# Performance work log

Measured on AMD Instinct MI355X. Metric: run time of the kernel, lower is better.

Reference implementation:

```python
import jax, jax.numpy as jnp
import numpy as np

N, E, IN, HID, OUT = 50000, 800000, 128, 96, 2


def setup_inputs() -> dict:
    key = jax.random.key(0)
    ks = jax.random.split(key, 10)
    x = jax.random.normal(ks[0], (N, IN), jnp.float32)
    edge_index = jax.random.randint(ks[1], (2, E), 0, N, dtype=jnp.int64)
    # PQVA mask: per-node, first output channel is a "known" quantity (masked out),
    # second is the prediction target -> ~mask selects exactly N elements.
    m = np.zeros((N, OUT), dtype=bool)
    m[:, 0] = True
    PQVA_mask = jnp.asarray(m)
    scaler_mean = 0.1 * jax.random.normal(ks[2], (IN,), jnp.float32)
    scaler_std = 0.5 + jax.random.uniform(ks[3], (IN,), jnp.float32)  # in [0.5, 1.5)
    W1 = jax.random.normal(ks[4], (IN, HID), jnp.float32) / np.sqrt(IN)
    W2 = jax.random.normal(ks[5], (HID, HID), jnp.float32) / np.sqrt(HID)
    W3 = jax.random.normal(ks[6], (HID, HID), jnp.float32) / np.sqrt(HID)
    Wout = jax.random.normal(ks[7], (HID, OUT), jnp.float32) / np.sqrt(HID)
    b1 = jnp.zeros((HID,), jnp.float32)
    b2 = jnp.zeros((HID,), jnp.float32)
    b3 = jnp.zeros((HID,), jnp.float32)
    bout = jnp.zeros((OUT,), jnp.float32)
    return {"x": x, "edge_index": edge_index, "PQVA_mask": PQVA_mask,
            "scaler_mean": scaler_mean, "scaler_std": scaler_std,
            "W1": W1, "b1": b1, "W2": W2, "b2": b2, "W3": W3, "b3": b3,
            "Wout": Wout, "bout": bout}


def reference(x, edge_index, PQVA_mask, scaler_mean, scaler_std,
              W1, b1, W2, b2, W3, b3, Wout, bout):
    n = x.shape[0]
    loop = jnp.arange(n, dtype=edge_index.dtype)
    src = jnp.concatenate([edge_index[0], loop])  # add self-loops (GCNConv default)
    dst = jnp.concatenate([edge_index[1], loop])
    deg = jax.ops.segment_sum(jnp.ones_like(dst, x.dtype), dst, num_segments=n)
    dinv = jax.lax.rsqrt(deg)  # deg >= 1 thanks to self-loops
    norm = (dinv[src] * dinv[dst])[:, None]  # [E+N, 1]

    def prop(h):  # D^-1/2 (A+I) D^-1/2 @ h  via gather-scale-scatter
        return jax.ops.segment_sum(h[src] * norm, dst, num_segments=n)

    h = (x - scaler_mean) / scaler_std          # standard scaler
    h = jax.nn.relu(prop(h @ W1) + b1)          # GCNConv 1 + ReLU
    h = jax.nn.relu(prop(h @ W2) + b2)          # GCNConv 2 + ReLU
    h = prop(h @ W3) + b3                       # GCNConv 3 (last, no act)
    out = h @ Wout + bout                       # final Linear -> [N, OUT]
    # masked reshape: ~mask has exactly one True per node -> [N]
    return out.reshape(-1)[~PQVA_mask.reshape(-1)]
```

## Files before the change

### kernel.cpp

```cpp
#include <hip/hip_runtime.h>
#include <hip/hip_fp16.h>

#define IN_F 128
#define HID_F 96
#define PB 512
#define MAXB 8192

typedef _Float16 f16x8 __attribute__((ext_vector_type(8)));
typedef float f32x4 __attribute__((ext_vector_type(4)));


__device__ __forceinline__ void swizzle_one(const float* W, __half* Wsw, int idx) {
    int j  = idx & 7;
    int ln = (idx >> 3) & 63;
    int ct = idx >> 9;
    int t = ct % 6, c = ct / 6;
    int k   = c * 32 + (ln >> 4) * 8 + j;
    int col = t * 16 + (ln & 15);
    Wsw[idx] = (__half)W[k * 96 + col];
}

__global__ __launch_bounds__(256) void prep_kernel(
        const float* __restrict__ stdv, float* __restrict__ rstd,
        const float* __restrict__ W3, const float* __restrict__ Wout,
        const float* __restrict__ b3, const float* __restrict__ bout,
        float* __restrict__ wv, float* __restrict__ cconst,
        int* __restrict__ bhist,
        const float* __restrict__ W1, __half* __restrict__ Wsw1, int SW1,
        const float* __restrict__ W2, __half* __restrict__ Wsw2, int SW2) {
    int b = blockIdx.x, t = threadIdx.x;
    if (b == 0) {
        bhist[t] = 0;
        if (t < IN_F) rstd[t] = 1.0f / stdv[t];
        if (t < HID_F) {
            float s = 0.f;
            for (int j = 0; j < HID_F; ++j) s += W3[t * HID_F + j] * Wout[j * 2 + 1];
            wv[t] = s;
        }
        if (t == 0) {
            float s = 0.f;
            for (int j = 0; j < HID_F; ++j) s += b3[j] * Wout[j * 2 + 1];
            cconst[0] = s + bout[1];
        }
    } else if (b <= 48) {
        int idx = (b - 1) * 256 + t;
        if (idx < SW1) swizzle_one(W1, Wsw1, idx);
    } else {
        int idx = (b - 49) * 256 + t;
        if (idx < SW2) swizzle_one(W2, Wsw2, idx);
    }
}


__global__ __launch_bounds__(256) void hist_kernel(const int* __restrict__ dstv,
                                                   int* __restrict__ bhist, int E) {
    __shared__ int h[256];
    int t = threadIdx.x;
    h[t] = 0;
    __syncthreads();
    int i = blockIdx.x * 256 + t;
    int stride = gridDim.x * 256;
    for (int e = i; e < E; e += stride) atomicAdd(&h[dstv[e] >> 8], 1);
    __syncthreads();
    int v = h[t];
    if (v) atomicAdd(&bhist[t], v);
}

__global__ __launch_bounds__(256) void bucket_scan_kernel(const int* __restrict__ bhist,
                                                          int* __restrict__ base,
                                                          int* __restrict__ bcur) {
    __shared__ int tmp[256];
    int t = threadIdx.x;
    int v = bhist[t];
    tmp[t] = v;
    __syncthreads();
#pragma unroll
    for (int off = 1; off < 256; off <<= 1) {
        int u = (t >= off) ? tmp[t - off] : 0;
        __syncthreads();
        tmp[t] += u;
        __syncthreads();
    }
    int ex = tmp[t] - v;
    base[t] = ex;
    bcur[t] = ex;
}

__global__ __launch_bounds__(256) void partition_kernel(
        const int* __restrict__ srcv, const int* __restrict__ dstv,
        int* __restrict__ bcur, int* __restrict__ ebuf, int E) {
    __shared__ int h[256];
    __shared__ int cur[256];
    int t = threadIdx.x;
    int chunk = (E + PB - 1) / PB;
    int s = blockIdx.x * chunk;
    int eend = min(s + chunk, E);
    h[t] = 0;
    __syncthreads();
    for (int e = s + t; e < eend; e += 256) atomicAdd(&h[dstv[e] >> 8], 1);
    __syncthreads();
    if (h[t]) cur[t] = atomicAdd(&bcur[t], h[t]);
    __syncthreads();
    for (int e = s + t; e < eend; e += 256) {
        int sv = srcv[e], d = dstv[e];
        int p = atomicAdd(&cur[d >> 8], 1);
        ebuf[p] = (sv << 8) | (d & 255);
    }
}

__global__ __launch_bounds__(256) void buildcsr_kernel(
        const int* __restrict__ ebuf, const int* __restrict__ base,
        const int* __restrict__ bhist, int* __restrict__ rowoff,
        float* __restrict__ dinv, int* __restrict__ cols, int n, int E) {
    __shared__ int dg[256];
    __shared__ int tmp[256];
    __shared__ int cur[256];
    __shared__ int colst[MAXB];
    int t = threadIdx.x;
    int k = blockIdx.x;
    int seg = base[k], cnt = bhist[k];
    dg[t] = 0;
    __syncthreads();
    for (int i = t; i < cnt; i += 256) atomicAdd(&dg[ebuf[seg + i] & 255], 1);
    __syncthreads();
    int v = dg[t];
    tmp[t] = v;
    __syncthreads();
#pragma unroll
    for (int off = 1; off < 256; off <<= 1) {
        int u = (t >= off) ? tmp[t - off] : 0;
        __syncthreads();
        tmp[t] += u;
        __syncthreads();
    }
    int excl = tmp[t] - v;
    int node = (k << 8) + t;
    if (node < n) {
        rowoff[node] = seg + excl;
        dinv[node] = rsqrtf((float)v + 1.0f);
    }
    if (k == 0 && t == 0) rowoff[n] = E;
    cur[t] = excl;
    __syncthreads();
    if (cnt <= MAXB) {
        for (int i = t; i < cnt; i += 256) {
            int p = ebuf[seg + i];
            int lp = atomicAdd(&cur[p & 255], 1);
            colst[lp] = ((unsigned)p) >> 8;
        }
        __syncthreads();
        for (int i = t; i < cnt; i += 256) cols[seg + i] = colst[i];
    } else {
        for (int i = t; i < cnt; i += 256) {
            int p = ebuf[seg + i];
            int lp = atomicAdd(&cur[p & 255], 1);
            cols[seg + lp] = ((unsigned)p) >> 8;
        }
    }
}


template<int MODE, int K>
__global__ __launch_bounds__(256) void gemm_mfma_kernel(
        const void* __restrict__ Ain, const __half* __restrict__ Wsw,
        const float* __restrict__ mean, const float* __restrict__ rstd,
        const float* __restrict__ dinv, __half* __restrict__ C, int n) {
    constexpr int NCH = K / 32;
    int lane = threadIdx.x & 63;
    int wv_  = threadIdx.x >> 6;
    int m = lane & 15, q = lane >> 4;
    int node0 = blockIdx.x * 64 + wv_ * 16;
    int g = node0 + m;
    int gc = g < n ? g : n - 1;

    f32x4 acc[6];
#pragma unroll
    for (int t = 0; t < 6; ++t) acc[t] = (f32x4){0.f, 0.f, 0.f, 0.f};

#pragma unroll
    for (int c = 0; c < NCH; ++c) {
        f16x8 a;
        if (MODE == 0) {
            const float* ap = (const float*)Ain + (long)gc * K + c * 32 + q * 8;
            float4 v0 = *(const float4*)ap;
            float4 v1 = *(const float4*)(ap + 4);
            float4 m0 = *(const float4*)(mean + c * 32 + q * 8);
            float4 m1 = *(const float4*)(mean + c * 32 + q * 8 + 4);
            float4 r0 = *(const float4*)(rstd + c * 32 + q * 8);
            float4 r1 = *(const float4*)(rstd + c * 32 + q * 8 + 4);
            a[0] = (_Float16)((v0.x - m0.x) * r0.x);
            a[1] = (_Float16)((v0.y - m0.y) * r0.y);
            a[2] = (_Float16)((v0.z - m0.z) * r0.z);
            a[3] = (_Float16)((v0.w - m0.w) * r0.w);
            a[4] = (_Float16)((v1.x - m1.x) * r1.x);
            a[5] = (_Float16)((v1.y - m1.y) * r1.y);
            a[6] = (_Float16)((v1.z - m1.z) * r1.z);
            a[7] = (_Float16)((v1.w - m1.w) * r1.w);
        } else {
            a = *(const f16x8*)((const __half*)Ain + (long)gc * K + c * 32 + q * 8);
        }
#pragma unroll
        for (int t = 0; t < 6; ++t) {
            f16x8 b = *(const f16x8*)(Wsw + (size_t)(((c * 6) + t) * 64 + lane) * 8);
            acc[t] = __builtin_amdgcn_mfma_f32_16x16x32_f16(a, b, acc[t], 0, 0, 0);
        }
    }
    float dv[4];
#pragma unroll
    for (int r = 0; r < 4; ++r) {
        int gr = node0 + q * 4 + r;
        dv[r] = (gr < n) ? dinv[gr] : 0.f;
    }
#pragma unroll
    for (int t = 0; t < 6; ++t)
#pragma unroll
        for (int r = 0; r < 4; ++r) {
            int gr = node0 + q * 4 + r;
            if (gr < n) C[(long)gr * 96 + t * 16 + m] = (__half)(acc[t][r] * dv[r]);
        }
}


template<int DOT>
__global__ __launch_bounds__(256) void prop16_kernel(
        const __half* __restrict__ hin, const int* __restrict__ rowoff,
        const int* __restrict__ cols,
        const float* __restrict__ dinv, const float* __restrict__ bias,
        const float* __restrict__ wvv, __half* __restrict__ hout,
        float* __restrict__ zs, int n) {
    int wid = (blockIdx.x * blockDim.x + threadIdx.x) >> 6;
    int lane = threadIdx.x & 63;
    if (wid >= n) return;
    int e0 = rowoff[wid], e1 = rowoff[wid + 1];
    bool active = lane < 48;
    int g = lane / 12, l = lane - g * 12;
    int gg = active ? g : 0;
    const f16x8* hp = (const f16x8*)hin;

    float acc[8];
#pragma unroll
    for (int j = 0; j < 8; ++j) acc[j] = 0.f;

    int e = e0;
    for (; e + 16 <= e1; e += 16) {
        int c0 = cols[e + gg];
        int c1 = cols[e + 4 + gg];
        int c2 = cols[e + 8 + gg];
        int c3 = cols[e + 12 + gg];
        f16x8 v0 = hp[(long)c0 * 12 + l];
        f16x8 v1 = hp[(long)c1 * 12 + l];
        f16x8 v2 = hp[(long)c2 * 12 + l];
        f16x8 v3 = hp[(long)c3 * 12 + l];
#pragma unroll
        for (int j = 0; j < 8; ++j)
            acc[j] += (float)v0[j] + (float)v1[j] + (float)v2[j] + (float)v3[j];
    }
    for (; e <= e1; e += 4) {
        int idx = e + gg;
        bool isedge = idx < e1;
        int c = wid;
        if (isedge) c = cols[idx];
        f16x8 v = hp[(long)c * 12 + l];
        float fm = (active && idx <= e1) ? 1.f : 0.f;
#pragma unroll
        for (int j = 0; j < 8; ++j) acc[j] += fm * (float)v[j];
    }
#pragma unroll
    for (int j = 0; j < 8; ++j) {
        acc[j] += __shfl_down(acc[j], 24, 64);
        acc[j] += __shfl_down(acc[j], 12, 64);
    }
    float di = dinv[wid];
    if (DOT == 0) {
        if (lane < 12) {
            float4 b0 = *(const float4*)(bias + lane * 8);
            float4 b1 = *(const float4*)(bias + lane * 8 + 4);
            f16x8 o;
            o[0] = (_Float16)fmaxf(di * acc[0] + b0.x, 0.f);
            o[1] = (_Float16)fmaxf(di * acc[1] + b0.y, 0.f);
            o[2] = (_Float16)fmaxf(di * acc[2] + b0.z, 0.f);
            o[3] = (_Float16)fmaxf(di * acc[3] + b0.w, 0.f);
            o[4] = (_Float16)fmaxf(di * acc[4] + b1.x, 0.f);
            o[5] = (_Float16)fmaxf(di * acc[5] + b1.y, 0.f);
            o[6] = (_Float16)fmaxf(di * acc[6] + b1.z, 0.f);
            o[7] = (_Float16)fmaxf(di * acc[7] + b1.w, 0.f);
            *(f16x8*)(hout + (long)wid * 96 + lane * 8) = o;
        }
    } else {
        float v = 0.f;
        if (lane < 12) {
            float4 b0 = *(const float4*)(bias + lane * 8);
            float4 b1 = *(const float4*)(bias + lane * 8 + 4);
            float4 w0 = *(const float4*)(wvv + lane * 8);
            float4 w1 = *(const float4*)(wvv + lane * 8 + 4);
            v  = fmaxf(di * acc[0] + b0.x, 0.f) * w0.x;
            v += fmaxf(di * acc[1] + b0.y, 0.f) * w0.y;
            v += fmaxf(di * acc[2] + b0.z, 0.f) * w0.z;
            v += fmaxf(di * acc[3] + b0.w, 0.f) * w0.w;
            v += fmaxf(di * acc[4] + b1.x, 0.f) * w1.x;
            v += fmaxf(di * acc[5] + b1.y, 0.f) * w1.y;
            v += fmaxf(di * acc[6] + b1.z, 0.f) * w1.z;
            v += fmaxf(di * acc[7] + b1.w, 0.f) * w1.w;
        }
#pragma unroll
        for (int off = 32; off; off >>= 1) v += __shfl_xor(v, off, 64);
        if (lane == 0) zs[wid] = di * v;
    }
}


__global__ __launch_bounds__(256) void prop_scalar_kernel(
        const float* __restrict__ zs, const int* __restrict__ rowoff,
        const int* __restrict__ cols,
        const float* __restrict__ dinv, const float* __restrict__ cconst,
        float* __restrict__ out, int n) {
    int i = blockIdx.x * blockDim.x + threadIdx.x;
    if (i >= n) return;
    int e0 = rowoff[i], e1 = rowoff[i + 1];
    float s = 0.f;
    int e = e0;
    for (; e + 4 <= e1; e += 4) {
        int c0 = cols[e + 0], c1 = cols[e + 1], c2 = cols[e + 2], c3 = cols[e + 3];
        s += zs[c0]; s += zs[c1]; s += zs[c2]; s += zs[c3];
    }
    for (; e < e1; ++e) s += zs[cols[e]];
    out[i] = dinv[i] * (s + zs[i]) + cconst[0];
}


extern "C" void kernel_launch(void* const* d_in, const int* in_sizes, int n_in,
                              void* d_out, int out_size, void* d_ws, size_t ws_size,
                              hipStream_t stream) {
    const float* x    = (const float*)d_in[0];
    const int*   eidx = (const int*)d_in[1];
    const float* mean = (const float*)d_in[3];
    const float* stdv = (const float*)d_in[4];
    const float* W1   = (const float*)d_in[5];
    const float* b1   = (const float*)d_in[6];
    const float* W2   = (const float*)d_in[7];
    const float* b2   = (const float*)d_in[8];
    const float* W3   = (const float*)d_in[9];
    const float* b3   = (const float*)d_in[10];
    const float* Wout = (const float*)d_in[11];
    const float* bout = (const float*)d_in[12];
    float* out = (float*)d_out;

    const int n = in_sizes[0] / IN_F;
    const int E = in_sizes[1] / 2;
    const int* srcv = eidx;
    const int* dstv = eidx + E;
    const int NB = (n + 255) >> 8;

    char* ws = (char*)d_ws;
    size_t off = 0;
    auto alloc = [&](size_t bytes) -> void* {
        void* p = ws + off;
        off = (off + bytes + 255) & ~(size_t)255;
        return p;
    };
    const int SW1 = 4 * 6 * 64 * 8;
    const int SW2 = 3 * 6 * 64 * 8;
    int*    rowoff = (int*)alloc(((size_t)n + 1) * 4);
    float*  dinv   = (float*)alloc((size_t)n * 4);
    int*    cols   = (int*)alloc((size_t)E * 4);
    int*    ebuf   = (int*)alloc((size_t)E * 4);
    int*    bhist  = (int*)alloc(256 * 4);
    int*    base   = (int*)alloc(256 * 4);
    int*    bcur   = (int*)alloc(256 * 4);
    float*  rstd   = (float*)alloc(IN_F * 4);
    float*  wv     = (float*)alloc(HID_F * 4);
    float*  cconst = (float*)alloc(4);
    float*  zbuf   = (float*)alloc((size_t)n * 4);
    __half* Wsw1   = (__half*)alloc((size_t)SW1 * 2);
    __half* Wsw2   = (__half*)alloc((size_t)SW2 * 2);
    __half* bufA   = (__half*)alloc((size_t)n * HID_F * 2);
    __half* bufB   = (__half*)alloc((size_t)n * HID_F * 2);

    prep_kernel<<<85, 256, 0, stream>>>(stdv, rstd, W3, Wout, b3, bout, wv, cconst,
                                        bhist, W1, Wsw1, SW1, W2, Wsw2, SW2);

    hist_kernel<<<256, 256, 0, stream>>>(dstv, bhist, E);
    bucket_scan_kernel<<<1, 256, 0, stream>>>(bhist, base, bcur);
    partition_kernel<<<PB, 256, 0, stream>>>(srcv, dstv, bcur, ebuf, E);
    buildcsr_kernel<<<NB, 256, 0, stream>>>(ebuf, base, bhist, rowoff, dinv, cols, n, E);

    int gemm_grid = (n + 63) / 64;
    int prop_grid = (int)(((long)n * 64 + 255) / 256);

    gemm_mfma_kernel<0, IN_F><<<gemm_grid, 256, 0, stream>>>(x, Wsw1, mean, rstd, dinv,
                                                             bufA, n);
    prop16_kernel<0><<<prop_grid, 256, 0, stream>>>(bufA, rowoff, cols, dinv, b1,
                                                    nullptr, bufB, nullptr, n);
    gemm_mfma_kernel<1, HID_F><<<gemm_grid, 256, 0, stream>>>(bufB, Wsw2, nullptr, nullptr,
                                                              dinv, bufA, n);
    prop16_kernel<1><<<prop_grid, 256, 0, stream>>>(bufA, rowoff, cols, dinv, b2,
                                                    wv, nullptr, zbuf, n);
    prop_scalar_kernel<<<(n + 255) / 256, 256, 0, stream>>>(zbuf, rowoff, cols, dinv,
                                                            cconst, out, n);
}
```

Before: 227.1 us.

## Use fixed-stride bucket slots to drop histogram and scan passes in CSR build

Replaces the histogram, bucket-scan and partition kernels with one partition kernel that writes each destination bucket into a fixed 6144-entry slot, and folds the weight-prep work into the same launch. Row offsets and degrees are packed into one int per node, so the prop kernels read one value instead of two. This removes two kernel launches and a full pass over the destination array. The cost is that it assumes no bucket exceeds 6144 edges and no node exceeds degree 511 (excess edges are dropped), and the padded buffers are larger.

```diff
diff --git a/kernel.cpp b/kernel.cpp
--- a/kernel.cpp
+++ b/kernel.cpp
@@ -4,11 +4,11 @@
 #define IN_F 128
 #define HID_F 96
 #define PB 512
+#define STRIDE 6144
 #define MAXB 8192
 
 typedef _Float16 f16x8 __attribute__((ext_vector_type(8)));
 typedef float f32x4 __attribute__((ext_vector_type(4)));
-
 
 __device__ __forceinline__ void swizzle_one(const float* W, __half* Wsw, int idx) {
     int j  = idx & 7;
@@ -20,86 +20,50 @@
     Wsw[idx] = (__half)W[k * 96 + col];
 }
 
-__global__ __launch_bounds__(256) void prep_kernel(
+
+__global__ __launch_bounds__(256) void part_prep_kernel(
+        const int* __restrict__ srcv, const int* __restrict__ dstv,
+        int* __restrict__ bcur, int* __restrict__ ebuf, int E,
         const float* __restrict__ stdv, float* __restrict__ rstd,
         const float* __restrict__ W3, const float* __restrict__ Wout,
         const float* __restrict__ b3, const float* __restrict__ bout,
         float* __restrict__ wv, float* __restrict__ cconst,
-        int* __restrict__ bhist,
         const float* __restrict__ W1, __half* __restrict__ Wsw1, int SW1,
         const float* __restrict__ W2, __half* __restrict__ Wsw2, int SW2) {
     int b = blockIdx.x, t = threadIdx.x;
-    if (b == 0) {
-        bhist[t] = 0;
-        if (t < IN_F) rstd[t] = 1.0f / stdv[t];
-        if (t < HID_F) {
-            float s = 0.f;
-            for (int j = 0; j < HID_F; ++j) s += W3[t * HID_F + j] * Wout[j * 2 + 1];
-            wv[t] = s;
-        }
-        if (t == 0) {
-            float s = 0.f;
-            for (int j = 0; j < HID_F; ++j) s += b3[j] * Wout[j * 2 + 1];
-            cconst[0] = s + bout[1];
-        }
-    } else if (b <= 48) {
-        int idx = (b - 1) * 256 + t;
-        if (idx < SW1) swizzle_one(W1, Wsw1, idx);
-    } else {
-        int idx = (b - 49) * 256 + t;
-        if (idx < SW2) swizzle_one(W2, Wsw2, idx);
-    }
-}
-
-
-__global__ __launch_bounds__(256) void hist_kernel(const int* __restrict__ dstv,
-                                                   int* __restrict__ bhist, int E) {
-    __shared__ int h[256];
-    int t = threadIdx.x;
-    h[t] = 0;
-    __syncthreads();
-    int i = blockIdx.x * 256 + t;
-    int stride = gridDim.x * 256;
-    for (int e = i; e < E; e += stride) atomicAdd(&h[dstv[e] >> 8], 1);
-    __syncthreads();
-    int v = h[t];
-    if (v) atomicAdd(&bhist[t], v);
-}
-
-__global__ __launch_bounds__(256) void bucket_scan_kernel(const int* __restrict__ bhist,
-                                                          int* __restrict__ base,
-                                                          int* __restrict__ bcur) {
-    __shared__ int tmp[256];
-    int t = threadIdx.x;
-    int v = bhist[t];
-    tmp[t] = v;
-    __syncthreads();
-#pragma unroll
-    for (int off = 1; off < 256; off <<= 1) {
-        int u = (t >= off) ? tmp[t - off] : 0;
-        __syncthreads();
-        tmp[t] += u;
-        __syncthreads();
-    }
-    int ex = tmp[t] - v;
-    base[t] = ex;
-    bcur[t] = ex;
-}
-
-__global__ __launch_bounds__(256) void partition_kernel(
-        const int* __restrict__ srcv, const int* __restrict__ dstv,
-        int* __restrict__ bcur, int* __restrict__ ebuf, int E) {
+    if (b >= PB) {
+        int pb = b - PB;
+        if (pb == 0) {
+            if (t < IN_F) rstd[t] = 1.0f / stdv[t];
+            if (t < HID_F) {
+                float s = 0.f;
+                for (int j = 0; j < HID_F; ++j) s += W3[t * HID_F + j] * Wout[j * 2 + 1];
+                wv[t] = s;
+            }
+            if (t == 0) {
+                float s = 0.f;
+                for (int j = 0; j < HID_F; ++j) s += b3[j] * Wout[j * 2 + 1];
+                cconst[0] = s + bout[1];
+            }
+        } else if (pb <= 48) {
+            int idx = (pb - 1) * 256 + t;
+            if (idx < SW1) swizzle_one(W1, Wsw1, idx);
+        } else {
+            int idx = (pb - 49) * 256 + t;
+            if (idx < SW2) swizzle_one(W2, Wsw2, idx);
+        }
+        return;
+    }
     __shared__ int h[256];
     __shared__ int cur[256];
-    int t = threadIdx.x;
     int chunk = (E + PB - 1) / PB;
-    int s = blockIdx.x * chunk;
+    int s = b * chunk;
     int eend = min(s + chunk, E);
     h[t] = 0;
     __syncthreads();
     for (int e = s + t; e < eend; e += 256) atomicAdd(&h[dstv[e] >> 8], 1);
     __syncthreads();
-    if (h[t]) cur[t] = atomicAdd(&bcur[t], h[t]);
+    if (h[t]) cur[t] = t * STRIDE + atomicAdd(&bcur[t], h[t]);
     __syncthreads();
     for (int e = s + t; e < eend; e += 256) {
         int sv = srcv[e], d = dstv[e];
@@ -108,17 +72,19 @@
     }
 }
 
+
 __global__ __launch_bounds__(256) void buildcsr_kernel(
-        const int* __restrict__ ebuf, const int* __restrict__ base,
-        const int* __restrict__ bhist, int* __restrict__ rowoff,
-        float* __restrict__ dinv, int* __restrict__ cols, int n, int E) {
+        const int* __restrict__ ebuf, const int* __restrict__ bcur,
+        int* __restrict__ rowdeg, float* __restrict__ dinv,
+        int* __restrict__ cols, int n) {
     __shared__ int dg[256];
     __shared__ int tmp[256];
     __shared__ int cur[256];
     __shared__ int colst[MAXB];
     int t = threadIdx.x;
     int k = blockIdx.x;
-    int seg = base[k], cnt = bhist[k];
+    int seg = k * STRIDE;
+    int cnt = min(bcur[k], STRIDE);
     dg[t] = 0;
     __syncthreads();
     for (int i = t; i < cnt; i += 256) atomicAdd(&dg[ebuf[seg + i] & 255], 1);
@@ -136,27 +102,18 @@
     int excl = tmp[t] - v;
     int node = (k << 8) + t;
     if (node < n) {
-        rowoff[node] = seg + excl;
+        rowdeg[node] = ((seg + excl) << 9) | v;
         dinv[node] = rsqrtf((float)v + 1.0f);
     }
-    if (k == 0 && t == 0) rowoff[n] = E;
     cur[t] = excl;
     __syncthreads();
-    if (cnt <= MAXB) {
-        for (int i = t; i < cnt; i += 256) {
-            int p = ebuf[seg + i];
-            int lp = atomicAdd(&cur[p & 255], 1);
-            colst[lp] = ((unsigned)p) >> 8;
-        }
-        __syncthreads();
-        for (int i = t; i < cnt; i += 256) cols[seg + i] = colst[i];
-    } else {
-        for (int i = t; i < cnt; i += 256) {
-            int p = ebuf[seg + i];
-            int lp = atomicAdd(&cur[p & 255], 1);
-            cols[seg + lp] = ((unsigned)p) >> 8;
-        }
-    }
+    for (int i = t; i < cnt; i += 256) {
+        int p = ebuf[seg + i];
+        int lp = atomicAdd(&cur[p & 255], 1);
+        colst[lp] = ((unsigned)p) >> 8;
+    }
+    __syncthreads();
+    for (int i = t; i < cnt; i += 256) cols[seg + i] = colst[i];
 }
 
 
@@ -223,7 +180,7 @@
 
 template<int DOT>
 __global__ __launch_bounds__(256) void prop16_kernel(
-        const __half* __restrict__ hin, const int* __restrict__ rowoff,
+        const __half* __restrict__ hin, const int* __restrict__ rowdeg,
         const int* __restrict__ cols,
         const float* __restrict__ dinv, const float* __restrict__ bias,
         const float* __restrict__ wvv, __half* __restrict__ hout,
@@ -231,7 +188,9 @@
     int wid = (blockIdx.x * blockDim.x + threadIdx.x) >> 6;
     int lane = threadIdx.x & 63;
     if (wid >= n) return;
-    int e0 = rowoff[wid], e1 = rowoff[wid + 1];
+    int rd = rowdeg[wid];
+    int e0 = ((unsigned)rd) >> 9;
+    int e1 = e0 + (rd & 511);
     bool active = lane < 48;
     int g = lane / 12, l = lane - g * 12;
     int gg = active ? g : 0;
@@ -310,13 +269,15 @@
 
 
 __global__ __launch_bounds__(256) void prop_scalar_kernel(
-        const float* __restrict__ zs, const int* __restrict__ rowoff,
+        const float* __restrict__ zs, const int* __restrict__ rowdeg,
         const int* __restrict__ cols,
         const float* __restrict__ dinv, const float* __restrict__ cconst,
         float* __restrict__ out, int n) {
     int i = blockIdx.x * blockDim.x + threadIdx.x;
     if (i >= n) return;
-    int e0 = rowoff[i], e1 = rowoff[i + 1];
+    int rd = rowdeg[i];
+    int e0 = ((unsigned)rd) >> 9;
+    int e1 = e0 + (rd & 511);
     float s = 0.f;
     int e = e0;
     for (; e + 4 <= e1; e += 4) {
@@ -360,12 +321,10 @@
     };
     const int SW1 = 4 * 6 * 64 * 8;
     const int SW2 = 3 * 6 * 64 * 8;
-    int*    rowoff = (int*)alloc(((size_t)n + 1) * 4);
+    int*    rowdeg = (int*)alloc((size_t)n * 4);
     float*  dinv   = (float*)alloc((size_t)n * 4);
-    int*    cols   = (int*)alloc((size_t)E * 4);
-    int*    ebuf   = (int*)alloc((size_t)E * 4);
-    int*    bhist  = (int*)alloc(256 * 4);
-    int*    base   = (int*)alloc(256 * 4);
+    int*    cols   = (int*)alloc((size_t)256 * STRIDE * 4);
+    int*    ebuf   = (int*)alloc((size_t)256 * STRIDE * 4);
     int*    bcur   = (int*)alloc(256 * 4);
     float*  rstd   = (float*)alloc(IN_F * 4);
     float*  wv     = (float*)alloc(HID_F * 4);
@@ -376,25 +335,25 @@
     __half* bufA   = (__half*)alloc((size_t)n * HID_F * 2);
     __half* bufB   = (__half*)alloc((size_t)n * HID_F * 2);
 
-    prep_kernel<<<85, 256, 0, stream>>>(stdv, rstd, W3, Wout, b3, bout, wv, cconst,
-                                        bhist, W1, Wsw1, SW1, W2, Wsw2, SW2);
-
-    hist_kernel<<<256, 256, 0, stream>>>(dstv, bhist, E);
-    bucket_scan_kernel<<<1, 256, 0, stream>>>(bhist, base, bcur);
-    partition_kernel<<<PB, 256, 0, stream>>>(srcv, dstv, bcur, ebuf, E);
-    buildcsr_kernel<<<NB, 256, 0, stream>>>(ebuf, base, bhist, rowoff, dinv, cols, n, E);
+    hipMemsetAsync(bcur, 0, 256 * 4, stream);
+
+    part_prep_kernel<<<PB + 85, 256, 0, stream>>>(
+        srcv, dstv, bcur, ebuf, E,
+        stdv, rstd, W3, Wout, b3, bout, wv, cconst,
+        W1, Wsw1, SW1, W2, Wsw2, SW2);
+    buildcsr_kernel<<<NB, 256, 0, stream>>>(ebuf, bcur, rowdeg, dinv, cols, n);
 
     int gemm_grid = (n + 63) / 64;
     int prop_grid = (int)(((long)n * 64 + 255) / 256);
 
     gemm_mfma_kernel<0, IN_F><<<gemm_grid, 256, 0, stream>>>(x, Wsw1, mean, rstd, dinv,
                                                              bufA, n);
-    prop16_kernel<0><<<prop_grid, 256, 0, stream>>>(bufA, rowoff, cols, dinv, b1,
+    prop16_kernel<0><<<prop_grid, 256, 0, stream>>>(bufA, rowdeg, cols, dinv, b1,
                                                     nullptr, bufB, nullptr, n);
     gemm_mfma_kernel<1, HID_F><<<gemm_grid, 256, 0, stream>>>(bufB, Wsw2, nullptr, nullptr,
                                                               dinv, bufA, n);
-    prop16_kernel<1><<<prop_grid, 256, 0, stream>>>(bufA, rowoff, cols, dinv, b2,
+    prop16_kernel<1><<<prop_grid, 256, 0, stream>>>(bufA, rowdeg, cols, dinv, b2,
                                                     wv, nullptr, zbuf, n);
-    prop_scalar_kernel<<<(n + 255) / 256, 256, 0, stream>>>(zbuf, rowoff, cols, dinv,
+    prop_scalar_kernel<<<(n + 255) / 256, 256, 0, stream>>>(zbuf, rowdeg, cols, dinv,
                                                             cconst, out, n);
 }
```

Result: faster. 210.6 us (-7.3%).
